# Kernel optimization log

Measured on AMD Instinct MI355X. Metric: run time of the kernel, lower is better.

The kernel has to match this reference:

```python
import jax, jax.numpy as jnp
import numpy as np

N_NODES = 50000
N_EDGES = 800000
D_IN = 128
D_OUT = 128


def setup_inputs() -> dict:
    key = jax.random.key(0)
    k1, k2, k3, k4 = jax.random.split(key, 4)
    input_feature = jax.random.normal(k1, (N_NODES, D_IN), dtype=jnp.float32)
    # COO sparse adjacency: edge_index[0]=row (dst), edge_index[1]=col (src)
    edge_index = jax.random.randint(k2, (2, N_EDGES), 0, N_NODES, dtype=jnp.int32)
    edge_weight = jax.random.uniform(k3, (N_EDGES,), dtype=jnp.float32)
    # kaiming-uniform-like init for weight; zeros bias (as in reset_parameters)
    bound = float(np.sqrt(6.0 / D_IN))
    weight = jax.random.uniform(k4, (D_IN, D_OUT), dtype=jnp.float32, minval=-bound, maxval=bound)
    bias = jnp.zeros((D_OUT,), dtype=jnp.float32)
    return {
        "input_feature": input_feature,
        "edge_index": edge_index,
        "edge_weight": edge_weight,
        "weight": weight,
        "bias": bias,
    }


def reference(input_feature, edge_index, edge_weight, weight, bias):
    # support = X @ W  -> [N, D_OUT]
    support = input_feature @ weight
    # sparse A @ support via gather + weighted segment_sum over destination rows
    row, col = edge_index[0], edge_index[1]
    msgs = support[col] * edge_weight[:, None]          # [E, D_OUT]
    output = jax.ops.segment_sum(msgs, row, num_segments=N_NODES)
    return output + bias
```

## Files before the change

kernel.cpp:

```cpp
#include <hip/hip_runtime.h>


#define N_NODES 50000
#define N_EDGES 800000
#define D 128
#define BROWS 66
#define NBUCKET 758
#define SLOT 1536
#define CHUNK 4096
#define EPT 16
#define GEMM_BLOCKS 782
#define PASS1_BLOCKS 196
#define CSTRIDE 16

typedef short bf16x8 __attribute__((ext_vector_type(8)));
typedef float f32x4 __attribute__((ext_vector_type(4)));

__device__ inline unsigned short f2bf(float f) {
    unsigned u = __float_as_uint(f);
    unsigned r = (u + 0x7FFFu + ((u >> 16) & 1u)) >> 16;
    return (unsigned short)r;
}


__global__ __launch_bounds__(256) void wprep_kernel(const float* __restrict__ W,
                                                    unsigned short* __restrict__ WT,
                                                    int* __restrict__ gcursor) {
    int idx = blockIdx.x * 256 + threadIdx.x;
    if (idx < 128 * 128) {
        int k = idx >> 7, n = idx & 127;
        WT[n * 136 + k] = f2bf(W[idx]);
    }
    if (idx < NBUCKET * CSTRIDE) gcursor[idx] = 0;
}

__global__ __launch_bounds__(256) void fused_kernel(const float* __restrict__ X,
                                                    const unsigned short* __restrict__ WT,
                                                    unsigned short* __restrict__ S16,
                                                    const int* __restrict__ ei,
                                                    const float* __restrict__ ew,
                                                    int* __restrict__ gcursor,
                                                    int2* __restrict__ staging) {
    __shared__ __align__(16) char shmem[52224];
    const int t = threadIdx.x;
    const int lane = t & 63, wid = t >> 6;

    if (blockIdx.x < GEMM_BLOCKS) {
        unsigned short* wt = (unsigned short*)shmem;
        unsigned short* xt = (unsigned short*)(shmem + 34816);
        const int row0 = blockIdx.x * 64;

        const uint4* WTg = (const uint4*)WT;
        uint4* wl = (uint4*)wt;
#pragma unroll
        for (int i = 0; i < 9; ++i) {
            int idx = t + 256 * i;
            if (idx < 2176) wl[idx] = WTg[idx];
        }
        const float4* X4 = (const float4*)X;
#pragma unroll
        for (int i = 0; i < 8; ++i) {
            int idx4 = t + 256 * i;
            int r = idx4 >> 5, c4 = idx4 & 31;
            int gr = row0 + r;
            float4 v = make_float4(0.f, 0.f, 0.f, 0.f);
            if (gr < N_NODES) v = X4[gr * 32 + c4];
            ushort4 u = make_ushort4(f2bf(v.x), f2bf(v.y), f2bf(v.z), f2bf(v.w));
            *(ushort4*)&xt[r * 136 + c4 * 4] = u;
        }
        __syncthreads();

        const int m = lane & 15;
        const int q = lane >> 4;
        const int rbase = wid * 16;

        f32x4 acc[8];
#pragma unroll
        for (int nt = 0; nt < 8; ++nt) acc[nt] = (f32x4){0.f, 0.f, 0.f, 0.f};
#pragma unroll
        for (int ks = 0; ks < 4; ++ks) {
            bf16x8 a = *(const bf16x8*)&xt[(rbase + m) * 136 + ks * 32 + q * 8];
#pragma unroll
            for (int nt = 0; nt < 8; ++nt) {
                bf16x8 b = *(const bf16x8*)&wt[(nt * 16 + m) * 136 + ks * 32 + q * 8];
                acc[nt] = __builtin_amdgcn_mfma_f32_16x16x32_bf16(a, b, acc[nt], 0, 0, 0);
            }
        }
        __syncthreads();
#pragma unroll
        for (int nt = 0; nt < 8; ++nt) {
            int col = nt * 16 + m;
#pragma unroll
            for (int r = 0; r < 4; ++r) {
                int rl = rbase + q * 4 + r;
                xt[rl * 136 + col] = f2bf(acc[nt][r]);
            }
        }
        __syncthreads();
#pragma unroll
        for (int i = 0; i < 4; ++i) {
            int id = t + 256 * i;
            int r = id >> 4, c8 = (id & 15) * 8;
            int gr = row0 + r;
            if (gr < N_NODES)
                *(uint4*)&S16[gr * 128 + c8] = *(const uint4*)&xt[r * 136 + c8];
        }
    } else {
        int* bufx            = (int*)shmem;
        int* bufw            = (int*)(shmem + 16384);
        unsigned short* bof  = (unsigned short*)(shmem + 32768);
        int* hist            = (int*)(shmem + 40960);
        int* lcur            = (int*)(shmem + 44032);
        int* bmg             = (int*)(shmem + 47104);
        int* wsum            = (int*)(shmem + 50176);
        const int base = (blockIdx.x - GEMM_BLOCKS) * CHUNK;

        hist[t] = 0;
        hist[t + 256] = 0;
        hist[t + 512] = 0;
        __syncthreads();

        int rows[EPT];
        int bkt[EPT];
#pragma unroll
        for (int i = 0; i < EPT; ++i) {
            int e = base + t + 256 * i;
            rows[i] = (e < N_EDGES) ? ei[e] : -1;
            bkt[i] = (rows[i] >= 0) ? (rows[i] / BROWS) : -1;
            if (bkt[i] >= 0) atomicAdd(&hist[bkt[i]], 1);
        }
        __syncthreads();

        int run = 0, exv[3], vv[3];
#pragma unroll
        for (int ph = 0; ph < 3; ++ph) {
            int v = hist[ph * 256 + t];
            vv[ph] = v;
            int incl = v;
#pragma unroll
            for (int off = 1; off < 64; off <<= 1) {
                int x = __shfl_up(incl, off, 64);
                if (lane >= off) incl += x;
            }
            if (lane == 63) wsum[wid] = incl;
            __syncthreads();
            int pre = 0, tot = 0;
#pragma unroll
            for (int w = 0; w < 4; ++w) {
                int x = wsum[w];
                if (w < wid) pre += x;
                tot += x;
            }
            exv[ph] = run + incl - v + pre;
            run += tot;
            __syncthreads();
        }
        const int total = run;
        lcur[t] = exv[0];
        lcur[t + 256] = exv[1];
        lcur[t + 512] = exv[2];
#pragma unroll
        for (int ph = 0; ph < 3; ++ph) {
            int b = ph * 256 + t;
            if (b < NBUCKET) {
                int v = vv[ph];
                if (v > 0) {
                    int gb = atomicAdd(&gcursor[b * CSTRIDE], v);
                    bmg[b] = b * SLOT + gb - exv[ph];
                }
            }
        }
        __syncthreads();

#pragma unroll
        for (int i = 0; i < EPT; ++i) {
            if (rows[i] >= 0) {
                int e = base + t + 256 * i;
                int col = ei[N_EDGES + e];
                float w = ew[e];
                int b = bkt[i];
                int lp = atomicAdd(&lcur[b], 1);
                int lrow = rows[i] - b * BROWS;
                bufx[lp] = (int)(((unsigned)lrow << 16) | (unsigned)col);
                bufw[lp] = __float_as_int(w);
                bof[lp] = (unsigned short)b;
            }
        }
        __syncthreads();

        for (int lp = t; lp < total; lp += 256) {
            int b = bof[lp];
            int g = bmg[b] + lp;
            if (g < (b + 1) * SLOT)
                staging[g] = make_int2(bufx[lp], bufw[lp]);
        }
    }
}

__global__ __launch_bounds__(512) void sortgather_kernel(const unsigned short* __restrict__ S16,
                                                         const int* __restrict__ gcursor,
                                                         const int2* __restrict__ staging,
                                                         const float* __restrict__ bias,
                                                         float* __restrict__ out) {
    __shared__ int2 in0[SLOT];
    __shared__ int2 in1[SLOT];
    __shared__ int hist[128];
    __shared__ int exs[128];
    __shared__ int lcur[128];
    __shared__ int wsum[2];
    const int t = threadIdx.x;
    const int b = blockIdx.x;
    const int lane = t & 63;
    int cnt = gcursor[b * CSTRIDE];
    if (cnt > SLOT) cnt = SLOT;

    if (t < 128) hist[t] = 0;
    __syncthreads();

    for (int i = t; i < cnt; i += 512) {
        int2 v = staging[b * SLOT + i];
        in0[i] = v;
        atomicAdd(&hist[((unsigned)v.x >> 16) & 127u], 1);
    }
    __syncthreads();

    int v = 0, incl = 0;
    if (t < 128) {
        v = hist[t];
        incl = v;
#pragma unroll
        for (int off = 1; off < 64; off <<= 1) {
            int x = __shfl_up(incl, off, 64);
            if (lane >= off) incl += x;
        }
        if (lane == 63) wsum[t >> 6] = incl;
    }
    __syncthreads();
    if (t < 128) {
        int pre = (t >= 64) ? wsum[0] : 0;
        int ex = incl - v + pre;
        exs[t] = ex;
        lcur[t] = ex;
    }
    __syncthreads();

    for (int i = t; i < cnt; i += 512) {
        int2 e = in0[i];
        int lr = (int)(((unsigned)e.x >> 16) & 127u);
        int p = atomicAdd(&lcur[lr], 1);
        in1[p] = e;
    }
    __syncthreads();

    const int wv = t >> 6;
    const int sub = lane >> 3;
    const int q = lane & 7;
    const uint4* S4 = (const uint4*)S16;
    const float4* bias4 = (const float4*)bias;
    float4 bb[4];
#pragma unroll
    for (int j = 0; j < 4; ++j) bb[j] = bias4[q * 4 + j];

    for (int rr = wv; rr < BROWS; rr += 8) {
        int beg = exs[rr];
        int end = beg + hist[rr];
        float acc[16];
#pragma unroll
        for (int i = 0; i < 16; ++i) acc[i] = 0.f;
        for (int p = beg + sub; p < end; p += 8) {
            int2 cw = in1[p];
            float w = __int_as_float(cw.y);
            int col = cw.x & 0xFFFF;
            uint4 v0 = S4[col * 16 + q * 2];
            uint4 v1 = S4[col * 16 + q * 2 + 1];
            acc[0]  += __uint_as_float(v0.x << 16) * w;
            acc[1]  += __uint_as_float(v0.x & 0xFFFF0000u) * w;
            acc[2]  += __uint_as_float(v0.y << 16) * w;
            acc[3]  += __uint_as_float(v0.y & 0xFFFF0000u) * w;
            acc[4]  += __uint_as_float(v0.z << 16) * w;
            acc[5]  += __uint_as_float(v0.z & 0xFFFF0000u) * w;
            acc[6]  += __uint_as_float(v0.w << 16) * w;
            acc[7]  += __uint_as_float(v0.w & 0xFFFF0000u) * w;
            acc[8]  += __uint_as_float(v1.x << 16) * w;
            acc[9]  += __uint_as_float(v1.x & 0xFFFF0000u) * w;
            acc[10] += __uint_as_float(v1.y << 16) * w;
            acc[11] += __uint_as_float(v1.y & 0xFFFF0000u) * w;
            acc[12] += __uint_as_float(v1.z << 16) * w;
            acc[13] += __uint_as_float(v1.z & 0xFFFF0000u) * w;
            acc[14] += __uint_as_float(v1.w << 16) * w;
            acc[15] += __uint_as_float(v1.w & 0xFFFF0000u) * w;
        }
#pragma unroll
        for (int i = 0; i < 16; ++i) acc[i] += __shfl_xor(acc[i], 8, 64);
#pragma unroll
        for (int i = 0; i < 16; ++i) acc[i] += __shfl_xor(acc[i], 16, 64);
#pragma unroll
        for (int i = 0; i < 16; ++i) acc[i] += __shfl_xor(acc[i], 32, 64);
        int gr = b * BROWS + rr;
        if (sub == 0 && gr < N_NODES) {
#pragma unroll
            for (int j = 0; j < 4; ++j) {
                float4 o = make_float4(acc[4 * j + 0] + bb[j].x, acc[4 * j + 1] + bb[j].y,
                                       acc[4 * j + 2] + bb[j].z, acc[4 * j + 3] + bb[j].w);
                ((float4*)out)[gr * 32 + q * 4 + j] = o;
            }
        }
    }
}

extern "C" void kernel_launch(void* const* d_in, const int* in_sizes, int n_in,
                              void* d_out, int out_size, void* d_ws, size_t ws_size,
                              hipStream_t stream) {
    const float* X    = (const float*)d_in[0];
    const int*   ei   = (const int*)d_in[1];
    const float* ew   = (const float*)d_in[2];
    const float* W    = (const float*)d_in[3];
    const float* bias = (const float*)d_in[4];
    float* out = (float*)d_out;

    char* ws = (char*)d_ws;
    unsigned short* S16 = (unsigned short*)(ws);
    int2* staging = (int2*)(ws + 12800000);
    int*  gcursor = (int*)(ws + 22114304);
    unsigned short* WT16 = (unsigned short*)(ws + 22162816);

    wprep_kernel<<<64, 256, 0, stream>>>(W, WT16, gcursor);
    fused_kernel<<<GEMM_BLOCKS + PASS1_BLOCKS, 256, 0, stream>>>(X, WT16, S16, ei, ew,
                                                                 gcursor, staging);
    sortgather_kernel<<<NBUCKET, 512, 0, stream>>>(S16, gcursor, staging, bias, out);
}
```

Measured before the change: 146.5 us.

## Replace bucketed LDS sort with per-row atomic slot staging and row-wise gather

The edge pass drops the per-block histogram, prefix scan and bucketed scatter. Each edge now takes a slot with a global atomicAdd on a per-row cursor and writes (col, weight) into a fixed 64-entry region for its row. The gather kernel then reads each row's edges directly, with no in-LDS counting sort, using 16 lanes per row and 4 edges in flight per wave. This removes the LDS sort and its barriers, but adds 800k random global atomics, a larger cursor array to zero and a larger, sparser staging buffer. It also silently drops edges for any row with more than 64 incoming edges.

```diff
diff --git a/kernel.cpp b/kernel.cpp
--- a/kernel.cpp
+++ b/kernel.cpp
@@ -4,14 +4,13 @@
 #define N_NODES 50000
 #define N_EDGES 800000
 #define D 128
-#define BROWS 66
-#define NBUCKET 758
-#define SLOT 1536
-#define CHUNK 4096
-#define EPT 16
+#define RSLOT 64
+#define CSTRIDE 16
 #define GEMM_BLOCKS 782
-#define PASS1_BLOCKS 196
-#define CSTRIDE 16
+#define SC_CHUNK 2048
+#define SC_BLOCKS 391
+#define GROWS 32
+#define GATHER_BLOCKS 1563
 
 typedef short bf16x8 __attribute__((ext_vector_type(8)));
 typedef float f32x4 __attribute__((ext_vector_type(4)));
@@ -31,7 +30,7 @@
         int k = idx >> 7, n = idx & 127;
         WT[n * 136 + k] = f2bf(W[idx]);
     }
-    if (idx < NBUCKET * CSTRIDE) gcursor[idx] = 0;
+    for (int i = idx; i < N_NODES * CSTRIDE; i += 512 * 256) gcursor[i] = 0;
 }
 
 __global__ __launch_bounds__(256) void fused_kernel(const float* __restrict__ X,
@@ -106,204 +105,74 @@
                 *(uint4*)&S16[gr * 128 + c8] = *(const uint4*)&xt[r * 136 + c8];
         }
     } else {
-        int* bufx            = (int*)shmem;
-        int* bufw            = (int*)(shmem + 16384);
-        unsigned short* bof  = (unsigned short*)(shmem + 32768);
-        int* hist            = (int*)(shmem + 40960);
-        int* lcur            = (int*)(shmem + 44032);
-        int* bmg             = (int*)(shmem + 47104);
-        int* wsum            = (int*)(shmem + 50176);
-        const int base = (blockIdx.x - GEMM_BLOCKS) * CHUNK;
-
-        hist[t] = 0;
-        hist[t + 256] = 0;
-        hist[t + 512] = 0;
-        __syncthreads();
-
-        int rows[EPT];
-        int bkt[EPT];
-#pragma unroll
-        for (int i = 0; i < EPT; ++i) {
+        const int base = (blockIdx.x - GEMM_BLOCKS) * SC_CHUNK;
+#pragma unroll
+        for (int i = 0; i < 8; ++i) {
             int e = base + t + 256 * i;
-            rows[i] = (e < N_EDGES) ? ei[e] : -1;
-            bkt[i] = (rows[i] >= 0) ? (rows[i] / BROWS) : -1;
-            if (bkt[i] >= 0) atomicAdd(&hist[bkt[i]], 1);
-        }
-        __syncthreads();
-
-        int run = 0, exv[3], vv[3];
-#pragma unroll
-        for (int ph = 0; ph < 3; ++ph) {
-            int v = hist[ph * 256 + t];
-            vv[ph] = v;
-            int incl = v;
-#pragma unroll
-            for (int off = 1; off < 64; off <<= 1) {
-                int x = __shfl_up(incl, off, 64);
-                if (lane >= off) incl += x;
-            }
-            if (lane == 63) wsum[wid] = incl;
-            __syncthreads();
-            int pre = 0, tot = 0;
-#pragma unroll
-            for (int w = 0; w < 4; ++w) {
-                int x = wsum[w];
-                if (w < wid) pre += x;
-                tot += x;
-            }
-            exv[ph] = run + incl - v + pre;
-            run += tot;
-            __syncthreads();
-        }
-        const int total = run;
-        lcur[t] = exv[0];
-        lcur[t + 256] = exv[1];
-        lcur[t + 512] = exv[2];
-#pragma unroll
-        for (int ph = 0; ph < 3; ++ph) {
-            int b = ph * 256 + t;
-            if (b < NBUCKET) {
-                int v = vv[ph];
-                if (v > 0) {
-                    int gb = atomicAdd(&gcursor[b * CSTRIDE], v);
-                    bmg[b] = b * SLOT + gb - exv[ph];
-                }
-            }
-        }
-        __syncthreads();
-
-#pragma unroll
-        for (int i = 0; i < EPT; ++i) {
-            if (rows[i] >= 0) {
-                int e = base + t + 256 * i;
+            if (e < N_EDGES) {
+                int row = ei[e];
                 int col = ei[N_EDGES + e];
                 float w = ew[e];
-                int b = bkt[i];
-                int lp = atomicAdd(&lcur[b], 1);
-                int lrow = rows[i] - b * BROWS;
-                bufx[lp] = (int)(((unsigned)lrow << 16) | (unsigned)col);
-                bufw[lp] = __float_as_int(w);
-                bof[lp] = (unsigned short)b;
+                int slot = atomicAdd(&gcursor[row * CSTRIDE], 1);
+                if (slot < RSLOT)
+                    staging[row * RSLOT + slot] = make_int2(col, __float_as_int(w));
             }
         }
-        __syncthreads();
-
-        for (int lp = t; lp < total; lp += 256) {
-            int b = bof[lp];
-            int g = bmg[b] + lp;
-            if (g < (b + 1) * SLOT)
-                staging[g] = make_int2(bufx[lp], bufw[lp]);
-        }
     }
 }
 
-__global__ __launch_bounds__(512) void sortgather_kernel(const unsigned short* __restrict__ S16,
-                                                         const int* __restrict__ gcursor,
-                                                         const int2* __restrict__ staging,
-                                                         const float* __restrict__ bias,
-                                                         float* __restrict__ out) {
-    __shared__ int2 in0[SLOT];
-    __shared__ int2 in1[SLOT];
-    __shared__ int hist[128];
-    __shared__ int exs[128];
-    __shared__ int lcur[128];
-    __shared__ int wsum[2];
+__global__ __launch_bounds__(256) void gather_kernel(const unsigned short* __restrict__ S16,
+                                                     const int* __restrict__ gcursor,
+                                                     const int2* __restrict__ staging,
+                                                     const float* __restrict__ bias,
+                                                     float* __restrict__ out) {
     const int t = threadIdx.x;
-    const int b = blockIdx.x;
+    const int wv = t >> 6;
     const int lane = t & 63;
-    int cnt = gcursor[b * CSTRIDE];
-    if (cnt > SLOT) cnt = SLOT;
-
-    if (t < 128) hist[t] = 0;
-    __syncthreads();
-
-    for (int i = t; i < cnt; i += 512) {
-        int2 v = staging[b * SLOT + i];
-        in0[i] = v;
-        atomicAdd(&hist[((unsigned)v.x >> 16) & 127u], 1);
-    }
-    __syncthreads();
-
-    int v = 0, incl = 0;
-    if (t < 128) {
-        v = hist[t];
-        incl = v;
-#pragma unroll
-        for (int off = 1; off < 64; off <<= 1) {
-            int x = __shfl_up(incl, off, 64);
-            if (lane >= off) incl += x;
-        }
-        if (lane == 63) wsum[t >> 6] = incl;
-    }
-    __syncthreads();
-    if (t < 128) {
-        int pre = (t >= 64) ? wsum[0] : 0;
-        int ex = incl - v + pre;
-        exs[t] = ex;
-        lcur[t] = ex;
-    }
-    __syncthreads();
-
-    for (int i = t; i < cnt; i += 512) {
-        int2 e = in0[i];
-        int lr = (int)(((unsigned)e.x >> 16) & 127u);
-        int p = atomicAdd(&lcur[lr], 1);
-        in1[p] = e;
-    }
-    __syncthreads();
-
-    const int wv = t >> 6;
-    const int sub = lane >> 3;
-    const int q = lane & 7;
+    const int sub = lane >> 4;
+    const int q = lane & 15;
     const uint4* S4 = (const uint4*)S16;
     const float4* bias4 = (const float4*)bias;
-    float4 bb[4];
-#pragma unroll
-    for (int j = 0; j < 4; ++j) bb[j] = bias4[q * 4 + j];
-
-    for (int rr = wv; rr < BROWS; rr += 8) {
-        int beg = exs[rr];
-        int end = beg + hist[rr];
-        float acc[16];
-#pragma unroll
-        for (int i = 0; i < 16; ++i) acc[i] = 0.f;
-        for (int p = beg + sub; p < end; p += 8) {
-            int2 cw = in1[p];
-            float w = __int_as_float(cw.y);
-            int col = cw.x & 0xFFFF;
-            uint4 v0 = S4[col * 16 + q * 2];
-            uint4 v1 = S4[col * 16 + q * 2 + 1];
-            acc[0]  += __uint_as_float(v0.x << 16) * w;
-            acc[1]  += __uint_as_float(v0.x & 0xFFFF0000u) * w;
-            acc[2]  += __uint_as_float(v0.y << 16) * w;
-            acc[3]  += __uint_as_float(v0.y & 0xFFFF0000u) * w;
-            acc[4]  += __uint_as_float(v0.z << 16) * w;
-            acc[5]  += __uint_as_float(v0.z & 0xFFFF0000u) * w;
-            acc[6]  += __uint_as_float(v0.w << 16) * w;
-            acc[7]  += __uint_as_float(v0.w & 0xFFFF0000u) * w;
-            acc[8]  += __uint_as_float(v1.x << 16) * w;
-            acc[9]  += __uint_as_float(v1.x & 0xFFFF0000u) * w;
-            acc[10] += __uint_as_float(v1.y << 16) * w;
-            acc[11] += __uint_as_float(v1.y & 0xFFFF0000u) * w;
-            acc[12] += __uint_as_float(v1.z << 16) * w;
-            acc[13] += __uint_as_float(v1.z & 0xFFFF0000u) * w;
-            acc[14] += __uint_as_float(v1.w << 16) * w;
-            acc[15] += __uint_as_float(v1.w & 0xFFFF0000u) * w;
-        }
-#pragma unroll
-        for (int i = 0; i < 16; ++i) acc[i] += __shfl_xor(acc[i], 8, 64);
-#pragma unroll
-        for (int i = 0; i < 16; ++i) acc[i] += __shfl_xor(acc[i], 16, 64);
-#pragma unroll
-        for (int i = 0; i < 16; ++i) acc[i] += __shfl_xor(acc[i], 32, 64);
-        int gr = b * BROWS + rr;
-        if (sub == 0 && gr < N_NODES) {
-#pragma unroll
-            for (int j = 0; j < 4; ++j) {
-                float4 o = make_float4(acc[4 * j + 0] + bb[j].x, acc[4 * j + 1] + bb[j].y,
-                                       acc[4 * j + 2] + bb[j].z, acc[4 * j + 3] + bb[j].w);
-                ((float4*)out)[gr * 32 + q * 4 + j] = o;
-            }
+    const float4 b0 = bias4[q * 2];
+    const float4 b1 = bias4[q * 2 + 1];
+    const int rbase = blockIdx.x * GROWS + wv * 8;
+
+    for (int r8 = 0; r8 < 8; ++r8) {
+        const int row = rbase + r8;
+        if (row >= N_NODES) break;
+        int cnt = gcursor[row * CSTRIDE];
+        if (cnt > RSLOT) cnt = RSLOT;
+
+        float acc[8];
+#pragma unroll
+        for (int i = 0; i < 8; ++i) acc[i] = 0.f;
+
+        for (int p = sub; p < cnt; p += 4) {
+            int2 e = staging[row * RSLOT + p];
+            float w = __int_as_float(e.y);
+            int col = e.x;
+            uint4 v = S4[col * 16 + q];
+            acc[0] += __uint_as_float(v.x << 16) * w;
+            acc[1] += __uint_as_float(v.x & 0xFFFF0000u) * w;
+            acc[2] += __uint_as_float(v.y << 16) * w;
+            acc[3] += __uint_as_float(v.y & 0xFFFF0000u) * w;
+            acc[4] += __uint_as_float(v.z << 16) * w;
+            acc[5] += __uint_as_float(v.z & 0xFFFF0000u) * w;
+            acc[6] += __uint_as_float(v.w << 16) * w;
+            acc[7] += __uint_as_float(v.w & 0xFFFF0000u) * w;
+        }
+#pragma unroll
+        for (int i = 0; i < 8; ++i) acc[i] += __shfl_xor(acc[i], 16, 64);
+#pragma unroll
+        for (int i = 0; i < 8; ++i) acc[i] += __shfl_xor(acc[i], 32, 64);
+
+        if (sub == 0) {
+            float4 o0 = make_float4(acc[0] + b0.x, acc[1] + b0.y,
+                                    acc[2] + b0.z, acc[3] + b0.w);
+            float4 o1 = make_float4(acc[4] + b1.x, acc[5] + b1.y,
+                                    acc[6] + b1.z, acc[7] + b1.w);
+            ((float4*)out)[row * 32 + q * 2] = o0;
+            ((float4*)out)[row * 32 + q * 2 + 1] = o1;
         }
     }
 }
@@ -321,11 +190,11 @@
     char* ws = (char*)d_ws;
     unsigned short* S16 = (unsigned short*)(ws);
     int2* staging = (int2*)(ws + 12800000);
-    int*  gcursor = (int*)(ws + 22114304);
-    unsigned short* WT16 = (unsigned short*)(ws + 22162816);
-
-    wprep_kernel<<<64, 256, 0, stream>>>(W, WT16, gcursor);
-    fused_kernel<<<GEMM_BLOCKS + PASS1_BLOCKS, 256, 0, stream>>>(X, WT16, S16, ei, ew,
-                                                                 gcursor, staging);
-    sortgather_kernel<<<NBUCKET, 512, 0, stream>>>(S16, gcursor, staging, bias, out);
-}
+    int*  gcursor = (int*)(ws + 38400000);
+    unsigned short* WT16 = (unsigned short*)(ws + 41600000);
+
+    wprep_kernel<<<512, 256, 0, stream>>>(W, WT16, gcursor);
+    fused_kernel<<<GEMM_BLOCKS + SC_BLOCKS, 256, 0, stream>>>(X, WT16, S16, ei, ew,
+                                                              gcursor, staging);
+    gather_kernel<<<GATHER_BLOCKS, 256, 0, stream>>>(S16, gcursor, staging, bias, out);
+}
```

New measurement: 167.1 us. 14.1% more time.

## Reorder fused kernel blocks and remap gather lanes to 16 per row

Applied to the files above, without the earlier changes.

The fused kernel now puts the edge-bucketing (pass1) blocks first and the GEMM blocks after them, so edge sorting is dispatched earlier. In the aggregation kernel each row is now handled by 16 lanes holding 8 features each, with 4 edges in flight per wave instead of 8 lanes holding 16 features. Each lane now issues one 16-byte gather per edge, the edge loop is unrolled by two, and one shuffle-reduction stage is dropped. This cuts accumulator registers in half and makes each gathered row fully coalesced across 16 lanes, but fewer edges are processed in parallel per wave.

```diff
diff --git a/kernel.cpp b/kernel.cpp
--- a/kernel.cpp
+++ b/kernel.cpp
@@ -22,6 +22,17 @@
     return (unsigned short)r;
 }
 
+__device__ inline void fma8(float* acc, uint4 v, float w) {
+    acc[0] += __uint_as_float(v.x << 16) * w;
+    acc[1] += __uint_as_float(v.x & 0xFFFF0000u) * w;
+    acc[2] += __uint_as_float(v.y << 16) * w;
+    acc[3] += __uint_as_float(v.y & 0xFFFF0000u) * w;
+    acc[4] += __uint_as_float(v.z << 16) * w;
+    acc[5] += __uint_as_float(v.z & 0xFFFF0000u) * w;
+    acc[6] += __uint_as_float(v.w << 16) * w;
+    acc[7] += __uint_as_float(v.w & 0xFFFF0000u) * w;
+}
+
 
 __global__ __launch_bounds__(256) void wprep_kernel(const float* __restrict__ W,
                                                     unsigned short* __restrict__ WT,
@@ -45,10 +56,10 @@
     const int t = threadIdx.x;
     const int lane = t & 63, wid = t >> 6;
 
-    if (blockIdx.x < GEMM_BLOCKS) {
+    if (blockIdx.x >= PASS1_BLOCKS) {
         unsigned short* wt = (unsigned short*)shmem;
         unsigned short* xt = (unsigned short*)(shmem + 34816);
-        const int row0 = blockIdx.x * 64;
+        const int row0 = (blockIdx.x - PASS1_BLOCKS) * 64;
 
         const uint4* WTg = (const uint4*)WT;
         uint4* wl = (uint4*)wt;
@@ -113,7 +124,7 @@
         int* lcur            = (int*)(shmem + 44032);
         int* bmg             = (int*)(shmem + 47104);
         int* wsum            = (int*)(shmem + 50176);
-        const int base = (blockIdx.x - GEMM_BLOCKS) * CHUNK;
+        const int base = blockIdx.x * CHUNK;
 
         hist[t] = 0;
         hist[t + 256] = 0;
@@ -253,57 +264,50 @@
     __syncthreads();
 
     const int wv = t >> 6;
-    const int sub = lane >> 3;
-    const int q = lane & 7;
+    const int sub = lane >> 4;
+    const int q = lane & 15;
     const uint4* S4 = (const uint4*)S16;
     const float4* bias4 = (const float4*)bias;
-    float4 bb[4];
-#pragma unroll
-    for (int j = 0; j < 4; ++j) bb[j] = bias4[q * 4 + j];
+    const float4 b0 = bias4[q * 2];
+    const float4 b1 = bias4[q * 2 + 1];
 
     for (int rr = wv; rr < BROWS; rr += 8) {
-        int beg = exs[rr];
-        int end = beg + hist[rr];
-        float acc[16];
-#pragma unroll
-        for (int i = 0; i < 16; ++i) acc[i] = 0.f;
-        for (int p = beg + sub; p < end; p += 8) {
+        const int beg = exs[rr];
+        const int end = beg + hist[rr];
+        float acc[8];
+#pragma unroll
+        for (int i = 0; i < 8; ++i) acc[i] = 0.f;
+
+        int p = beg + sub;
+        for (; p + 4 < end; p += 8) {
+            int2 cw0 = in1[p];
+            int2 cw1 = in1[p + 4];
+            uint4 v0 = S4[(cw0.x & 0xFFFF) * 16 + q];
+            uint4 v1 = S4[(cw1.x & 0xFFFF) * 16 + q];
+            float w0 = __int_as_float(cw0.y);
+            float w1 = __int_as_float(cw1.y);
+            fma8(acc, v0, w0);
+            fma8(acc, v1, w1);
+        }
+        if (p < end) {
             int2 cw = in1[p];
+            uint4 v2 = S4[(cw.x & 0xFFFF) * 16 + q];
             float w = __int_as_float(cw.y);
-            int col = cw.x & 0xFFFF;
-            uint4 v0 = S4[col * 16 + q * 2];
-            uint4 v1 = S4[col * 16 + q * 2 + 1];
-            acc[0]  += __uint_as_float(v0.x << 16) * w;
-            acc[1]  += __uint_as_float(v0.x & 0xFFFF0000u) * w;
-            acc[2]  += __uint_as_float(v0.y << 16) * w;
-            acc[3]  += __uint_as_float(v0.y & 0xFFFF0000u) * w;
-            acc[4]  += __uint_as_float(v0.z << 16) * w;
-            acc[5]  += __uint_as_float(v0.z & 0xFFFF0000u) * w;
-            acc[6]  += __uint_as_float(v0.w << 16) * w;
-            acc[7]  += __uint_as_float(v0.w & 0xFFFF0000u) * w;
-            acc[8]  += __uint_as_float(v1.x << 16) * w;
-            acc[9]  += __uint_as_float(v1.x & 0xFFFF0000u) * w;
-            acc[10] += __uint_as_float(v1.y << 16) * w;
-            acc[11] += __uint_as_float(v1.y & 0xFFFF0000u) * w;
-            acc[12] += __uint_as_float(v1.z << 16) * w;
-            acc[13] += __uint_as_float(v1.z & 0xFFFF0000u) * w;
-            acc[14] += __uint_as_float(v1.w << 16) * w;
-            acc[15] += __uint_as_float(v1.w & 0xFFFF0000u) * w;
-        }
-#pragma unroll
-        for (int i = 0; i < 16; ++i) acc[i] += __shfl_xor(acc[i], 8, 64);
-#pragma unroll
-        for (int i = 0; i < 16; ++i) acc[i] += __shfl_xor(acc[i], 16, 64);
-#pragma unroll
-        for (int i = 0; i < 16; ++i) acc[i] += __shfl_xor(acc[i], 32, 64);
+            fma8(acc, v2, w);
+        }
+#pragma unroll
+        for (int i = 0; i < 8; ++i) acc[i] += __shfl_xor(acc[i], 16, 64);
+#pragma unroll
+        for (int i = 0; i < 8; ++i) acc[i] += __shfl_xor(acc[i], 32, 64);
+
         int gr = b * BROWS + rr;
         if (sub == 0 && gr < N_NODES) {
-#pragma unroll
-            for (int j = 0; j < 4; ++j) {
-                float4 o = make_float4(acc[4 * j + 0] + bb[j].x, acc[4 * j + 1] + bb[j].y,
-                                       acc[4 * j + 2] + bb[j].z, acc[4 * j + 3] + bb[j].w);
-                ((float4*)out)[gr * 32 + q * 4 + j] = o;
-            }
+            float4 o0 = make_float4(acc[0] + b0.x, acc[1] + b0.y,
+                                    acc[2] + b0.z, acc[3] + b0.w);
+            float4 o1 = make_float4(acc[4] + b1.x, acc[5] + b1.y,
+                                    acc[6] + b1.z, acc[7] + b1.w);
+            ((float4*)out)[gr * 32 + q * 2] = o0;
+            ((float4*)out)[gr * 32 + q * 2 + 1] = o1;
         }
     }
 }
```

After: 133.2 us. 1.1x faster.
